# Optimization experiments

Measured on AMD Instinct MI355X. Metric: run time of the kernel, lower is better.

## Reference

```python
import jax, jax.numpy as jnp
import numpy as np

ORDER = 256
THETA = 1024.0
HIDDEN = 512
FEAT = 128
BATCH = 64
SEQ = 1025  # loop consumes steps 1..SEQ-1 -> T = 1024 outputs
LEAKY_SLOPE = 0.2  # tf.nn.leaky_relu default alpha


def _expm_np(M):
    # scaling-and-squaring + Taylor, float64, sufficient for the LMU A matrix
    n = max(0, int(np.ceil(np.log2(max(1.0, np.linalg.norm(M, 1))))) + 4)
    A = M / (2.0 ** n)
    E = np.eye(M.shape[0])
    term = np.eye(M.shape[0])
    for k in range(1, 24):
        term = term @ A / k
        E = E + term
    for _ in range(n):
        E = E @ E
    return E


def get_state_space_matrices(order, theta):
    Q = np.arange(order, dtype=np.float64)
    R = (2 * Q + 1)[:, None] / theta
    j, i = np.meshgrid(Q, Q)
    Ac = np.where(i < j, -1, (-1.0) ** (i - j + 1)) * R
    Bc = (-1.0) ** Q[:, None] * R
    # zero-order-hold discretization with dt=1 (matches scipy cont2discrete zoh)
    Ad = _expm_np(Ac)
    Bd = np.linalg.solve(Ac, (Ad - np.eye(order)) @ Bc)
    return Ad.astype(np.float32), Bd.astype(np.float32)


def _glorot(key, shape):
    fan_in, fan_out = shape[0], shape[1]
    lim = np.sqrt(6.0 / (fan_in + fan_out))
    return jax.random.uniform(key, shape, jnp.float32, -lim, lim)


def setup_inputs() -> dict:
    key = jax.random.key(0)
    ks = jax.random.split(key, 6)
    A_np, B_np = get_state_space_matrices(ORDER, THETA)
    return {
        "x": jax.random.normal(ks[0], (BATCH, SEQ, FEAT), jnp.float32),
        "A": jnp.asarray(A_np),            # (order, order)
        "Bv": jnp.asarray(B_np),           # (order, 1)
        "W_x": _glorot(ks[1], (FEAT, HIDDEN)),
        "e_x": _glorot(ks[2], (FEAT, 1)),
        "W_h": _glorot(ks[3], (HIDDEN, HIDDEN)),
        "W_m": _glorot(ks[4], (HIDDEN, ORDER)),
    }


def reference(x, A, Bv, W_x, e_x, W_h, W_m):
    B, S, F = x.shape
    order = A.shape[0]
    hidden_dim = W_h.shape[0]
    b_row = Bv[:, 0]  # (order,)

    def step(carry, x_t):
        m, h = carry                       # m: (B, order), h: (B, hidden)
        u = x_t @ e_x                      # (B, 1)
        m = m @ A.T + b_row[None, :] * u   # A@m + B*u  -> (B, order)
        h = x_t @ W_x + h @ W_h.T + m @ W_m.T
        h = jnp.where(h >= 0, h, LEAKY_SLOPE * h)  # leaky_relu(alpha=0.2)
        return (m, h), h

    m0 = jnp.zeros((B, order), jnp.float32)
    h0 = jnp.zeros((B, hidden_dim), jnp.float32)
    xs = jnp.swapaxes(x[:, 1:, :], 0, 1)   # (T, B, F); step 0 is skipped as in the source
    _, hs = jax.lax.scan(step, (m0, h0), xs)
    return jnp.swapaxes(hs, 0, 1)          # (B, T, hidden)
```

## Files before the change

kernel.cpp:

```cpp
#include <hip/hip_runtime.h>
#include <stdint.h>


typedef _Float16 half8 __attribute__((ext_vector_type(8)));
typedef float f32x4 __attribute__((ext_vector_type(4)));
typedef unsigned int u32x4 __attribute__((ext_vector_type(4)));
typedef unsigned int u32x2 __attribute__((ext_vector_type(2)));

union H8 { half8 h; unsigned int u[4]; };
union F16 { u32x4 q; half8 h; };

#define MFMA16(a, b, c) __builtin_amdgcn_mfma_f32_16x16x32_f16((a), (b), (c), 0, 0, 0)
#define ASTORE64(p, v) __hip_atomic_store((unsigned long long*)(p), (v), \
                                          __ATOMIC_RELAXED, __HIP_MEMORY_SCOPE_AGENT)

__device__ __forceinline__ half8 ld_frag16(const _Float16* W, size_t foff) {
    F16 r;
    r.q = *(const u32x4*)(W + foff);
    return r.h;
}

__device__ __forceinline__ void unpack8(u32x4 A, u32x4 B, half8& hi, half8& lo) {
    H8 h, l;
    h.u[0] = (A[0] & 0xffffu) | (A[1] << 16);  l.u[0] = (A[0] >> 16) | (A[1] & 0xffff0000u);
    h.u[1] = (A[2] & 0xffffu) | (A[3] << 16);  l.u[1] = (A[2] >> 16) | (A[3] & 0xffff0000u);
    h.u[2] = (B[0] & 0xffffu) | (B[1] << 16);  l.u[2] = (B[0] >> 16) | (B[1] & 0xffff0000u);
    h.u[3] = (B[2] & 0xffffu) | (B[3] << 16);  l.u[3] = (B[2] >> 16) | (B[3] & 0xffff0000u);
    hi = h.h; lo = l.h;
}

__global__ void k_prep(const float* __restrict__ A, const float* __restrict__ W_x,
                       const float* __restrict__ W_h, const float* __restrict__ W_m,
                       _Float16* __restrict__ Whi, _Float16* __restrict__ Wlo,
                       _Float16* __restrict__ WxThi, _Float16* __restrict__ WxTlo,
                       float* __restrict__ WmT, float* __restrict__ AT) {
    int bid = blockIdx.x, tid = threadIdx.x;
    if (bid < 512) {
        int r = bid;
        for (int c = tid; c < 512; c += 256) {
            float v = W_h[(size_t)r * 512 + c];
            _Float16 hi = (_Float16)v;
            _Float16 lo = (_Float16)(v - (float)hi);
            int cb = c >> 5, w = c & 31;
            int kgi = (w & 15) >> 2;
            int e = (w & 3) + ((w & 16) ? 4 : 0);
            size_t idx = (((size_t)r * 16 + cb) * 4 + kgi) * 8 + e;
            Whi[idx] = hi;
            Wlo[idx] = lo;
        }
    } else if (bid < 1024) {
        int n = bid - 512;
        if (tid < 128) {
            int f = tid;
            float v = W_x[(size_t)f * 512 + n];
            _Float16 hi = (_Float16)v;
            _Float16 lo = (_Float16)(v - (float)hi);
            int kt = f >> 5, w = f & 31;
            int kgi = (w & 15) >> 2;
            int e = (w & 3) + ((w & 16) ? 4 : 0);
            size_t idx = (((size_t)n * 4 + kt) * 4 + kgi) * 8 + e;
            WxThi[idx] = hi;
            WxTlo[idx] = lo;
        }
    } else if (bid < 1280) {
        int d = bid - 1024;
        for (int n = tid; n < 512; n += 256)
            WmT[(size_t)d * 512 + n] = W_m[(size_t)n * 256 + d];
    } else {
        int e = bid - 1280;
        if (tid < 256) AT[(size_t)e * 256 + tid] = A[(size_t)tid * 256 + e];
    }
}

__global__ void k_u(const float* __restrict__ x, const float* __restrict__ e_x,
                    float* __restrict__ u) {
    int wave = threadIdx.x >> 6, l = threadIdx.x & 63;
    int t = blockIdx.x * 4 + wave;
    int b = blockIdx.y;
    const float* xr = x + ((size_t)b * 1025 + t + 1) * 128;
    float s = xr[2 * l] * e_x[2 * l] + xr[2 * l + 1] * e_x[2 * l + 1];
#pragma unroll
    for (int off = 1; off < 64; off <<= 1) s += __shfl_xor(s, off);
    if (l == 0) u[(size_t)b * 1024 + t] = s;
}

__global__ void k_a64(const float* __restrict__ S, float* __restrict__ D,
                      float* __restrict__ DT, int writeT) {
    int r = blockIdx.x, c = threadIdx.x;
    float acc = 0.f;
    for (int e = 0; e < 256; ++e)
        acc += S[(size_t)r * 256 + e] * S[(size_t)e * 256 + c];
    D[(size_t)r * 256 + c] = acc;
    if (writeT) DT[(size_t)c * 256 + r] = acc;
}

__global__ void k_vk(const float* __restrict__ AT, const float* __restrict__ Bv,
                     float* __restrict__ V) {
    __shared__ float cur[256];
    int tid = threadIdx.x;
    cur[tid] = Bv[tid];
    V[tid] = cur[tid];
    __syncthreads();
    for (int k = 1; k < 64; ++k) {
        float nv = 0.f;
        for (int e = 0; e < 256; ++e) nv += AT[(size_t)e * 256 + tid] * cur[e];
        __syncthreads();
        cur[tid] = nv;
        V[(size_t)k * 256 + tid] = nv;
        __syncthreads();
    }
}

__global__ void k_vchain(const float* __restrict__ A64T, float* __restrict__ V) {
    __shared__ float cur[256];
    int j = blockIdx.x, d = threadIdx.x;
    cur[d] = V[(size_t)j * 256 + d];
    __syncthreads();
    for (int c = 1; c < 16; ++c) {
        float nv = 0.f;
        for (int e = 0; e < 256; ++e) nv += A64T[(size_t)e * 256 + d] * cur[e];
        __syncthreads();
        cur[d] = nv;
        V[((size_t)c * 64 + j) * 256 + d] = nv;
        __syncthreads();
    }
}

__global__ void k_c(const float* __restrict__ V, const float* __restrict__ WmT,
                    _Float16* __restrict__ CThi) {
    int k = blockIdx.x, n = threadIdx.x;
    const float* vk = V + (size_t)k * 256;
    float acc = 0.f;
    for (int d = 0; d < 256; ++d) acc += vk[d] * WmT[(size_t)d * 512 + n];
    int ck = k >> 5, w = k & 31;
    int kgi = (w & 15) >> 2;
    int e = (w & 3) + ((w & 16) ? 4 : 0);
    CThi[(((size_t)n * 32 + ck) * 4 + kgi) * 8 + e] = (_Float16)acc;
}

__global__ __launch_bounds__(256, 1) void k_preconv(const float* __restrict__ x,
                                                    const float* __restrict__ u,
                                                    const _Float16* __restrict__ WxThi,
                                                    const _Float16* __restrict__ WxTlo,
                                                    const _Float16* __restrict__ CThi,
                                                    float* __restrict__ out) {
    __shared__ float xt[64][132];
    __shared__ float ut[1088];
    int tid = threadIdx.x;
    int Mb = blockIdx.x, Nb = blockIdx.y;
    int b = Mb >> 4;
    int t0 = (Mb & 15) * 64;
    const float* src = x + ((size_t)b * 1025 + t0 + 1) * 128;
#pragma unroll
    for (int i = 0; i < 8; ++i) {
        int idx = tid + i * 256;
        int row = idx >> 5, c4 = (idx & 31) * 4;
        *(f32x4*)&xt[row][c4] = *(const f32x4*)(src + (size_t)row * 128 + c4);
    }
    for (int i = tid; i < 1088; i += 256) {
        int tau = t0 - 1024 + i;
        ut[i] = (tau >= 0) ? u[(size_t)b * 1024 + tau] : 0.f;
    }
    __syncthreads();

    int wave = tid >> 6, l = tid & 63;
    int kg4 = l >> 4, kg = kg4 * 4;
    int mrow = wave * 16 + (l & 15);

    half8 ah[4], al[4];
#pragma unroll
    for (int kt = 0; kt < 4; ++kt) {
        f32x4 f0 = *(const f32x4*)&xt[mrow][kt * 32 + kg];
        f32x4 f1 = *(const f32x4*)&xt[mrow][kt * 32 + kg + 16];
        H8 hh, ll;
#pragma unroll
        for (int e = 0; e < 4; ++e) {
            _Float16 h0 = (_Float16)f0[e];
            ((_Float16*)&hh)[e] = h0;
            ((_Float16*)&ll)[e] = (_Float16)(f0[e] - (float)h0);
            _Float16 h1 = (_Float16)f1[e];
            ((_Float16*)&hh)[e + 4] = h1;
            ((_Float16*)&ll)[e + 4] = (_Float16)(f1[e] - (float)h1);
        }
        ah[kt] = hh.h;
        al[kt] = ll.h;
    }

    f32x4 acc[16];
#pragma unroll
    for (int nt = 0; nt < 16; ++nt) acc[nt] = (f32x4)0.f;

#pragma unroll
    for (int nt = 0; nt < 16; ++nt) {
        size_t nrow = (size_t)(Nb * 256 + nt * 16 + (l & 15));
#pragma unroll
        for (int kt = 0; kt < 4; ++kt) {
            size_t fo = (((nrow * 4 + kt) * 4 + kg4)) * 8;
            half8 bh = ld_frag16(WxThi, fo);
            half8 bl = ld_frag16(WxTlo, fo);
            acc[nt] = MFMA16(ah[kt], bh, acc[nt]);
            acc[nt] = MFMA16(al[kt], bh, acc[nt]);
            acc[nt] = MFMA16(ah[kt], bl, acc[nt]);
        }
    }

    for (int ck = 0; ck < 32; ++ck) {
        int base0 = mrow + 1024 - ck * 32 - kg;
        H8 au;
#pragma unroll
        for (int e = 0; e < 4; ++e) {
            ((_Float16*)&au)[e] = (_Float16)ut[base0 - e];
            ((_Float16*)&au)[e + 4] = (_Float16)ut[base0 - 16 - e];
        }
#pragma unroll
        for (int nt = 0; nt < 16; ++nt) {
            size_t nrow = (size_t)(Nb * 256 + nt * 16 + (l & 15));
            half8 bh = ld_frag16(CThi, (((nrow * 32 + ck) * 4 + kg4)) * 8);
            acc[nt] = MFMA16(au.h, bh, acc[nt]);
        }
    }

#pragma unroll
    for (int nt = 0; nt < 16; ++nt) {
#pragma unroll
        for (int r = 0; r < 4; ++r) {
            size_t bt = (size_t)Mb * 64 + wave * 16 + 4 * (l >> 4) + r;
            out[bt * 512 + Nb * 256 + nt * 16 + (l & 15)] = acc[nt][r];
        }
    }
}

#define TSTATE_U32 (64 * 512 * 2)

#define LD8W(p, v0, v1, v2, v3, v4, v5, v6, v7)                                   \
    asm volatile("global_load_dwordx4 %0, %8, off\n\t"                            \
                 "global_load_dwordx4 %1, %8, off offset:64\n\t"                  \
                 "global_load_dwordx4 %2, %8, off offset:128\n\t"                 \
                 "global_load_dwordx4 %3, %8, off offset:192\n\t"                 \
                 "global_load_dwordx4 %4, %8, off offset:256\n\t"                 \
                 "global_load_dwordx4 %5, %8, off offset:320\n\t"                 \
                 "global_load_dwordx4 %6, %8, off offset:384\n\t"                 \
                 "global_load_dwordx4 %7, %8, off offset:448"                     \
                 : "=&v"(v0), "=&v"(v1), "=&v"(v2), "=&v"(v3), "=&v"(v4),         \
                   "=&v"(v5), "=&v"(v6), "=&v"(v7)                                \
                 : "v"(p))

#define ISSUE_STATE(p)                                                            \
    asm volatile("global_load_dwordx4 %0, %8, off sc1\n\t"                        \
                 "global_load_dwordx4 %1, %8, off offset:512 sc1\n\t"             \
                 "global_load_dwordx4 %2, %8, off offset:1024 sc1\n\t"            \
                 "global_load_dwordx4 %3, %8, off offset:1536 sc1\n\t"            \
                 "global_load_dwordx4 %4, %8, off offset:2048 sc1\n\t"            \
                 "global_load_dwordx4 %5, %8, off offset:2560 sc1\n\t"            \
                 "global_load_dwordx4 %6, %8, off offset:3072 sc1\n\t"            \
                 "global_load_dwordx4 %7, %8, off offset:3584 sc1"                \
                 : "=&v"(e0), "=&v"(e1), "=&v"(e2), "=&v"(e3),                    \
                   "=&v"(e4), "=&v"(e5), "=&v"(e6), "=&v"(e7)                     \
                 : "v"(p) : "memory")

#define VM0_FENCE()                                                               \
    do {                                                                          \
        asm volatile("s_waitcnt vmcnt(0)" ::: "memory");                          \
        __builtin_amdgcn_sched_barrier(0);                                        \
    } while (0)

#define TAGBAD(exp)                                                               \
    ((e0[1] ^ (exp)) | (e0[3] ^ (exp)) | (e1[1] ^ (exp)) | (e1[3] ^ (exp)) |      \
     (e2[1] ^ (exp)) | (e2[3] ^ (exp)) | (e3[1] ^ (exp)) | (e3[3] ^ (exp)) |      \
     (e4[1] ^ (exp)) | (e4[3] ^ (exp)) | (e5[1] ^ (exp)) | (e5[3] ^ (exp)) |      \
     (e6[1] ^ (exp)) | (e6[3] ^ (exp)) | (e7[1] ^ (exp)) | (e7[3] ^ (exp)))

#define BC8(x) __builtin_bit_cast(half8, x)

__global__ __launch_bounds__(512, 1) void k_seq(const _Float16* __restrict__ Whi,
                                                const _Float16* __restrict__ Wlo,
                                                unsigned int* sbuf, float* out) {
    __shared__ unsigned int sval[16 * 512];
    __shared__ f32x4 pex[8][64];
    int tid = threadIdx.x;
    int w = tid >> 6, l = tid & 63;
    int g = blockIdx.x >> 3, rank = blockIdx.x & 7;
    int kh = w >> 2;
    int kbase = kh * 256;
    int kg4 = l >> 4, kg = kg4 * 4;

    u32x4 wh0, wh1, wh2, wh3, wh4, wh5, wh6, wh7;
    u32x4 wl0, wl1, wl2, wl3, wl4, wl5, wl6, wl7;
    int frow = rank * 64 + (w & 3) * 16 + (l & 15);
    {
        size_t fo = (((size_t)frow * 16 + kh * 8) * 4 + kg4) * 8;
        LD8W(Whi + fo, wh0, wh1, wh2, wh3, wh4, wh5, wh6, wh7);
        LD8W(Wlo + fo, wl0, wl1, wl2, wl3, wl4, wl5, wl6, wl7);
        asm volatile("s_waitcnt vmcnt(0)" ::: "memory");
    }

    int bX = ((l & 15) & 7) << 2;
    int bloc = 2 * w + (l >> 5);
    unsigned int sX = (unsigned int)((bloc & 7) << 2);
    int lam = l & 31;
    size_t soff = (size_t)(g * 16 + bloc) * 1024 + (size_t)lam * 4;

    u32x4 e0, e1, e2, e3, e4, e5, e6, e7;
    ISSUE_STATE(sbuf + soff);

#pragma unroll 1
    for (int t = 1; t <= 1024; ++t) {
        float pxw0, pxw1;
        {
            int r0 = 2 * kh;
            int bG0 = g * 16 + 4 * (l >> 4) + r0;
            pxw0 = out[(((size_t)bG0 << 10) + (t - 1)) * 512 + frow];
            pxw1 = out[(((size_t)(bG0 + 1) << 10) + (t - 1)) * 512 + frow];
        }

        const unsigned int* pL = sbuf + (size_t)((t - 1) & 1) * TSTATE_U32 + soff;
        unsigned int exp = (unsigned int)(t - 1);
        VM0_FENCE();
        unsigned int bad = TAGBAD(exp);
        int rounds = 0;
        while (!__all(bad == 0)) {
            if (++rounds > 200000) break;
            ISSUE_STATE(pL);
            VM0_FENCE();
            bad = TAGBAD(exp);
        }

        {
            unsigned int* row = sval + bloc * 512;
            int kb = 2 * lam;
            *(u32x2*)&row[(kb)       ^ sX] = (u32x2){e0[0], e0[2]};
            *(u32x2*)&row[(kb + 64)  ^ sX] = (u32x2){e1[0], e1[2]};
            *(u32x2*)&row[(kb + 128) ^ sX] = (u32x2){e2[0], e2[2]};
            *(u32x2*)&row[(kb + 192) ^ sX] = (u32x2){e3[0], e3[2]};
            *(u32x2*)&row[(kb + 256) ^ sX] = (u32x2){e4[0], e4[2]};
            *(u32x2*)&row[(kb + 320) ^ sX] = (u32x2){e5[0], e5[2]};
            *(u32x2*)&row[(kb + 384) ^ sX] = (u32x2){e6[0], e6[2]};
            *(u32x2*)&row[(kb + 448) ^ sX] = (u32x2){e7[0], e7[2]};
        }
        __syncthreads();

        const unsigned int* brow = sval + (l & 15) * 512;
        f32x4 acc = (f32x4)0.f;
#define RSTEP(KT, BH, BL)                                                         \
        {                                                                         \
            int k0 = kbase + (KT) * 32 + kg;                                      \
            u32x4 qa = *(const u32x4*)&brow[k0 ^ bX];                             \
            u32x4 qb = *(const u32x4*)&brow[(k0 + 16) ^ bX];                      \
            half8 Ah, Al;                                                         \
            unpack8(qa, qb, Ah, Al);                                              \
            acc = MFMA16(Ah, BC8(BH), acc);                                       \
            acc = MFMA16(Al, BC8(BH), acc);                                       \
            acc = MFMA16(Ah, BC8(BL), acc);                                       \
        }
        RSTEP(0, wh0, wl0);
        RSTEP(1, wh1, wl1);
        RSTEP(2, wh2, wl2);
        RSTEP(3, wh3, wl3);
        RSTEP(4, wh4, wl4);
        RSTEP(5, wh5, wl5);
        RSTEP(6, wh6, wl6);
        RSTEP(7, wh7, wl7);
#undef RSTEP

        pex[w][l] = acc;
        __syncthreads();
        f32x4 sum = acc + pex[w ^ 4][l];

        float s0 = kh ? sum[2] : sum[0];
        float s1 = kh ? sum[3] : sum[1];
        unsigned int* wbuf = sbuf + (size_t)(t & 1) * TSTATE_U32;
        int bG0 = g * 16 + 4 * (l >> 4) + 2 * kh;
        float v0 = s0 + pxw0;
        v0 = (v0 >= 0.f) ? v0 : 0.2f * v0;
        float v1 = s1 + pxw1;
        v1 = (v1 >= 0.f) ? v1 : 0.2f * v1;
        {
            _Float16 hi0 = (_Float16)v0, lo0 = (_Float16)(v0 - (float)hi0);
            _Float16 hi1 = (_Float16)v1, lo1 = (_Float16)(v1 - (float)hi1);
            unsigned int p0 = (unsigned int)__builtin_bit_cast(unsigned short, hi0) |
                              ((unsigned int)__builtin_bit_cast(unsigned short, lo0) << 16);
            unsigned int p1 = (unsigned int)__builtin_bit_cast(unsigned short, hi1) |
                              ((unsigned int)__builtin_bit_cast(unsigned short, lo1) << 16);
            unsigned long long t64 = (unsigned long long)(unsigned int)t << 32;
            ASTORE64(wbuf + ((size_t)bG0 * 512 + frow) * 2, (unsigned long long)p0 | t64);
            ASTORE64(wbuf + ((size_t)(bG0 + 1) * 512 + frow) * 2,
                     (unsigned long long)p1 | t64);
        }
        ISSUE_STATE(sbuf + (size_t)(t & 1) * TSTATE_U32 + soff);
        out[(((size_t)bG0 << 10) + (t - 1)) * 512 + frow] = v0;
        out[(((size_t)(bG0 + 1) << 10) + (t - 1)) * 512 + frow] = v1;
    }
}

extern "C" void kernel_launch(void* const* d_in, const int* in_sizes, int n_in,
                              void* d_out, int out_size, void* d_ws, size_t ws_size,
                              hipStream_t stream) {
    const float* x   = (const float*)d_in[0];
    const float* A   = (const float*)d_in[1];
    const float* Bv  = (const float*)d_in[2];
    const float* W_x = (const float*)d_in[3];
    const float* e_x = (const float*)d_in[4];
    const float* W_h = (const float*)d_in[5];
    const float* W_m = (const float*)d_in[6];
    float* out = (float*)d_out;

    char* ws = (char*)d_ws;
    size_t off = 0;
    auto carve = [&](size_t n) -> char* {
        char* p = ws + off;
        off += (n + 255) & ~(size_t)255;
        return p;
    };
    _Float16* Whi   = (_Float16*)carve(512 * 512 * 2);
    _Float16* Wlo   = (_Float16*)carve(512 * 512 * 2);
    _Float16* WxThi = (_Float16*)carve(512 * 128 * 2);
    _Float16* WxTlo = (_Float16*)carve(512 * 128 * 2);
    float* WmT      = (float*)carve(256 * 512 * 4);
    float* AT       = (float*)carve(256 * 256 * 4);
    float* u        = (float*)carve(64 * 1024 * 4);
    unsigned int* sbuf = (unsigned int*)carve((size_t)2 * TSTATE_U32 * 4);
    float* Apw0     = (float*)carve(256 * 256 * 4);
    float* Apw1     = (float*)carve(256 * 256 * 4);
    float* A64T     = (float*)carve(256 * 256 * 4);
    float* V        = (float*)carve(1024 * 256 * 4);
    _Float16* CThi  = (_Float16*)carve(512 * 1024 * 2);

    hipMemsetAsync(sbuf, 0, (size_t)2 * TSTATE_U32 * 4, stream);

    hipLaunchKernelGGL(k_prep, dim3(1536), dim3(256), 0, stream, A, W_x, W_h, W_m,
                       Whi, Wlo, WxThi, WxTlo, WmT, AT);
    hipLaunchKernelGGL(k_u, dim3(256, 64), dim3(256), 0, stream, x, e_x, u);

    hipLaunchKernelGGL(k_a64, dim3(256), dim3(256), 0, stream, A, Apw0, A64T, 0);
    hipLaunchKernelGGL(k_a64, dim3(256), dim3(256), 0, stream, Apw0, Apw1, A64T, 0);
    hipLaunchKernelGGL(k_a64, dim3(256), dim3(256), 0, stream, Apw1, Apw0, A64T, 0);
    hipLaunchKernelGGL(k_a64, dim3(256), dim3(256), 0, stream, Apw0, Apw1, A64T, 0);
    hipLaunchKernelGGL(k_a64, dim3(256), dim3(256), 0, stream, Apw1, Apw0, A64T, 0);
    hipLaunchKernelGGL(k_a64, dim3(256), dim3(256), 0, stream, Apw0, Apw1, A64T, 1);

    hipLaunchKernelGGL(k_vk, dim3(1), dim3(256), 0, stream, AT, Bv, V);
    hipLaunchKernelGGL(k_vchain, dim3(64), dim3(256), 0, stream, A64T, V);
    hipLaunchKernelGGL(k_c, dim3(1024), dim3(512), 0, stream, V, WmT, CThi);

    hipLaunchKernelGGL(k_preconv, dim3(1024, 2), dim3(256), 0, stream, x, u,
                       WxThi, WxTlo, CThi, out);

    void* args[] = {(void*)&Whi, (void*)&Wlo, (void*)&sbuf, (void*)&out};
    hipLaunchCooperativeKernel((void*)k_seq, dim3(32), dim3(512), args, 0, stream);
}
```

Baseline: 5.217 ms.

## Replace serial A^k·B chain with power-doubling and retile the C precompute

The single-block serial 63-step chain computing A^k·B is replaced by log-depth doubling. Each stage multiplies the existing vectors by a saved transposed power of A (A^2, A^4, …), so every A^(2^i) is now stored along with its transpose. The W_m transpose pass is removed, and k_c is rewritten so each block stages 8 rows of W_m in shared memory and reuses them across 1024 k vectors with vector loads. The intent is to shorten the serial precompute critical path before the main kernels, at the cost of more launches and more workspace.

```diff
diff --git a/kernel.cpp b/kernel.cpp
--- a/kernel.cpp
+++ b/kernel.cpp
@@ -29,11 +29,11 @@
     hi = h.h; lo = l.h;
 }
 
-__global__ void k_prep(const float* __restrict__ A, const float* __restrict__ W_x,
-                       const float* __restrict__ W_h, const float* __restrict__ W_m,
+__global__ void k_prep(const float* __restrict__ A, const float* __restrict__ Bv,
+                       const float* __restrict__ W_x, const float* __restrict__ W_h,
                        _Float16* __restrict__ Whi, _Float16* __restrict__ Wlo,
                        _Float16* __restrict__ WxThi, _Float16* __restrict__ WxTlo,
-                       float* __restrict__ WmT, float* __restrict__ AT) {
+                       float* __restrict__ AT, float* __restrict__ V) {
     int bid = blockIdx.x, tid = threadIdx.x;
     if (bid < 512) {
         int r = bid;
@@ -63,12 +63,10 @@
             WxTlo[idx] = lo;
         }
     } else if (bid < 1280) {
-        int d = bid - 1024;
-        for (int n = tid; n < 512; n += 256)
-            WmT[(size_t)d * 512 + n] = W_m[(size_t)n * 256 + d];
+        int e = bid - 1024;
+        if (tid < 256) AT[(size_t)e * 256 + tid] = A[(size_t)tid * 256 + e];
     } else {
-        int e = bid - 1280;
-        if (tid < 256) AT[(size_t)e * 256 + tid] = A[(size_t)tid * 256 + e];
+        if (tid < 256) V[tid] = Bv[tid];
     }
 }
 
@@ -85,30 +83,24 @@
 }
 
 __global__ void k_a64(const float* __restrict__ S, float* __restrict__ D,
-                      float* __restrict__ DT, int writeT) {
+                      float* __restrict__ DT) {
     int r = blockIdx.x, c = threadIdx.x;
     float acc = 0.f;
     for (int e = 0; e < 256; ++e)
         acc += S[(size_t)r * 256 + e] * S[(size_t)e * 256 + c];
     D[(size_t)r * 256 + c] = acc;
-    if (writeT) DT[(size_t)c * 256 + r] = acc;
-}
-
-__global__ void k_vk(const float* __restrict__ AT, const float* __restrict__ Bv,
-                     float* __restrict__ V) {
+    DT[(size_t)c * 256 + r] = acc;
+}
+
+__global__ void k_vdouble(const float* __restrict__ PT, float* __restrict__ V,
+                          int base) {
     __shared__ float cur[256];
-    int tid = threadIdx.x;
-    cur[tid] = Bv[tid];
-    V[tid] = cur[tid];
+    int j0 = blockIdx.x, d = threadIdx.x;
+    cur[d] = V[(size_t)j0 * 256 + d];
     __syncthreads();
-    for (int k = 1; k < 64; ++k) {
-        float nv = 0.f;
-        for (int e = 0; e < 256; ++e) nv += AT[(size_t)e * 256 + tid] * cur[e];
-        __syncthreads();
-        cur[tid] = nv;
-        V[(size_t)k * 256 + tid] = nv;
-        __syncthreads();
-    }
+    float acc = 0.f;
+    for (int e = 0; e < 256; ++e) acc += PT[(size_t)e * 256 + d] * cur[e];
+    V[(size_t)(base + j0) * 256 + d] = acc;
 }
 
 __global__ void k_vchain(const float* __restrict__ A64T, float* __restrict__ V) {
@@ -126,16 +118,35 @@
     }
 }
 
-__global__ void k_c(const float* __restrict__ V, const float* __restrict__ WmT,
+__global__ void k_c(const float* __restrict__ V, const float* __restrict__ W_m,
                     _Float16* __restrict__ CThi) {
-    int k = blockIdx.x, n = threadIdx.x;
-    const float* vk = V + (size_t)k * 256;
-    float acc = 0.f;
-    for (int d = 0; d < 256; ++d) acc += vk[d] * WmT[(size_t)d * 512 + n];
-    int ck = k >> 5, w = k & 31;
-    int kgi = (w & 15) >> 2;
-    int e = (w & 3) + ((w & 16) ? 4 : 0);
-    CThi[(((size_t)n * 32 + ck) * 4 + kgi) * 8 + e] = (_Float16)acc;
+    __shared__ float wm[8][260];
+    int bid = blockIdx.x, tid = threadIdx.x;
+    for (int i = tid; i < 8 * 256; i += 256)
+        wm[i >> 8][i & 255] = W_m[(size_t)(bid * 8 + (i >> 8)) * 256 + (i & 255)];
+    __syncthreads();
+    for (int j = 0; j < 4; ++j) {
+        int k = tid + 256 * j;
+        const f32x4* vk = (const f32x4*)(V + (size_t)k * 256);
+        float a[8];
+#pragma unroll
+        for (int n = 0; n < 8; ++n) a[n] = 0.f;
+        for (int d4 = 0; d4 < 64; ++d4) {
+            f32x4 vv = vk[d4];
+#pragma unroll
+            for (int n = 0; n < 8; ++n)
+                a[n] += vv[0] * wm[n][d4 * 4] + vv[1] * wm[n][d4 * 4 + 1] +
+                        vv[2] * wm[n][d4 * 4 + 2] + vv[3] * wm[n][d4 * 4 + 3];
+        }
+        int ck = k >> 5, w = k & 31;
+        int kgi = (w & 15) >> 2;
+        int e = (w & 3) + ((w & 16) ? 4 : 0);
+#pragma unroll
+        for (int n = 0; n < 8; ++n) {
+            size_t nn = (size_t)(bid * 8 + n);
+            CThi[((nn * 32 + ck) * 4 + kgi) * 8 + e] = (_Float16)a[n];
+        }
+    }
 }
 
 __global__ __launch_bounds__(256, 1) void k_preconv(const float* __restrict__ x,
@@ -415,32 +426,45 @@
     _Float16* Wlo   = (_Float16*)carve(512 * 512 * 2);
     _Float16* WxThi = (_Float16*)carve(512 * 128 * 2);
     _Float16* WxTlo = (_Float16*)carve(512 * 128 * 2);
-    float* WmT      = (float*)carve(256 * 512 * 4);
     float* AT       = (float*)carve(256 * 256 * 4);
     float* u        = (float*)carve(64 * 1024 * 4);
     unsigned int* sbuf = (unsigned int*)carve((size_t)2 * TSTATE_U32 * 4);
-    float* Apw0     = (float*)carve(256 * 256 * 4);
-    float* Apw1     = (float*)carve(256 * 256 * 4);
-    float* A64T     = (float*)carve(256 * 256 * 4);
+    float* P2   = (float*)carve(256 * 256 * 4);
+    float* P4   = (float*)carve(256 * 256 * 4);
+    float* P8   = (float*)carve(256 * 256 * 4);
+    float* P16  = (float*)carve(256 * 256 * 4);
+    float* P32  = (float*)carve(256 * 256 * 4);
+    float* P64  = (float*)carve(256 * 256 * 4);
+    float* P2T  = (float*)carve(256 * 256 * 4);
+    float* P4T  = (float*)carve(256 * 256 * 4);
+    float* P8T  = (float*)carve(256 * 256 * 4);
+    float* P16T = (float*)carve(256 * 256 * 4);
+    float* P32T = (float*)carve(256 * 256 * 4);
+    float* A64T = (float*)carve(256 * 256 * 4);
     float* V        = (float*)carve(1024 * 256 * 4);
     _Float16* CThi  = (_Float16*)carve(512 * 1024 * 2);
 
     hipMemsetAsync(sbuf, 0, (size_t)2 * TSTATE_U32 * 4, stream);
 
-    hipLaunchKernelGGL(k_prep, dim3(1536), dim3(256), 0, stream, A, W_x, W_h, W_m,
-                       Whi, Wlo, WxThi, WxTlo, WmT, AT);
+    hipLaunchKernelGGL(k_prep, dim3(1281), dim3(256), 0, stream, A, Bv, W_x, W_h,
+                       Whi, Wlo, WxThi, WxTlo, AT, V);
     hipLaunchKernelGGL(k_u, dim3(256, 64), dim3(256), 0, stream, x, e_x, u);
 
-    hipLaunchKernelGGL(k_a64, dim3(256), dim3(256), 0, stream, A, Apw0, A64T, 0);
-    hipLaunchKernelGGL(k_a64, dim3(256), dim3(256), 0, stream, Apw0, Apw1, A64T, 0);
-    hipLaunchKernelGGL(k_a64, dim3(256), dim3(256), 0, stream, Apw1, Apw0, A64T, 0);
-    hipLaunchKernelGGL(k_a64, dim3(256), dim3(256), 0, stream, Apw0, Apw1, A64T, 0);
-    hipLaunchKernelGGL(k_a64, dim3(256), dim3(256), 0, stream, Apw1, Apw0, A64T, 0);
-    hipLaunchKernelGGL(k_a64, dim3(256), dim3(256), 0, stream, Apw0, Apw1, A64T, 1);
-
-    hipLaunchKernelGGL(k_vk, dim3(1), dim3(256), 0, stream, AT, Bv, V);
+    hipLaunchKernelGGL(k_a64, dim3(256), dim3(256), 0, stream, A, P2, P2T);
+    hipLaunchKernelGGL(k_a64, dim3(256), dim3(256), 0, stream, P2, P4, P4T);
+    hipLaunchKernelGGL(k_a64, dim3(256), dim3(256), 0, stream, P4, P8, P8T);
+    hipLaunchKernelGGL(k_a64, dim3(256), dim3(256), 0, stream, P8, P16, P16T);
+    hipLaunchKernelGGL(k_a64, dim3(256), dim3(256), 0, stream, P16, P32, P32T);
+    hipLaunchKernelGGL(k_a64, dim3(256), dim3(256), 0, stream, P32, P64, A64T);
+
+    hipLaunchKernelGGL(k_vdouble, dim3(1), dim3(256), 0, stream, AT, V, 1);
+    hipLaunchKernelGGL(k_vdouble, dim3(2), dim3(256), 0, stream, P2T, V, 2);
+    hipLaunchKernelGGL(k_vdouble, dim3(4), dim3(256), 0, stream, P4T, V, 4);
+    hipLaunchKernelGGL(k_vdouble, dim3(8), dim3(256), 0, stream, P8T, V, 8);
+    hipLaunchKernelGGL(k_vdouble, dim3(16), dim3(256), 0, stream, P16T, V, 16);
+    hipLaunchKernelGGL(k_vdouble, dim3(32), dim3(256), 0, stream, P32T, V, 32);
     hipLaunchKernelGGL(k_vchain, dim3(64), dim3(256), 0, stream, A64T, V);
-    hipLaunchKernelGGL(k_c, dim3(1024), dim3(512), 0, stream, V, WmT, CThi);
+    hipLaunchKernelGGL(k_c, dim3(64), dim3(256), 0, stream, V, W_m, CThi);
 
     hipLaunchKernelGGL(k_preconv, dim3(1024, 2), dim3(256), 0, stream, x, u,
                        WxThi, WxTlo, CThi, out);
```

Result: faster. 5.093 ms (-2.4%).
